# Kernel tuning notes

Measured on AMD Instinct MI355X. Metric: run time of the kernel, lower is better.

## Reference

```python
import jax, jax.numpy as jnp
import numpy as np

IN_CH, OUT_CH, HEAD, QK_DIM, V_DIM = 256, 256, 8, 512, 512


def setup_inputs() -> dict:
    key = jax.random.key(0)
    ks = jax.random.split(key, 5)
    B, H, W = 16, 32, 32
    x = jax.random.normal(ks[0], (B, IN_CH, H, W), dtype=jnp.float32)
    # 1x1 conv weights stored as [out_ch, in_ch]
    qkv_out = 2 * QK_DIM + V_DIM
    qkv_w = jax.random.normal(ks[1], (qkv_out, IN_CH), dtype=jnp.float32) * (IN_CH ** -0.5)
    qkv_b = jax.random.normal(ks[2], (qkv_out,), dtype=jnp.float32) * 0.02
    proj_w = jax.random.normal(ks[3], (OUT_CH, V_DIM), dtype=jnp.float32) * (V_DIM ** -0.5)
    proj_b = jax.random.normal(ks[4], (OUT_CH,), dtype=jnp.float32) * 0.02
    return {"x": x, "qkv_w": qkv_w, "qkv_b": qkv_b, "proj_w": proj_w, "proj_b": proj_b}


def reference(x, qkv_w, qkv_b, proj_w, proj_b):
    B, C, H, W = x.shape
    N = H * W
    dh = QK_DIM // HEAD
    dv = V_DIM // HEAD
    scale = dh ** -0.5
    # 1x1 conv == channel GEMM
    qkv = jnp.einsum('bchw,oc->bohw', x, qkv_w) + qkv_b[None, :, None, None]
    q, k, v = jnp.split(qkv, [QK_DIM, 2 * QK_DIM], axis=1)
    # [B, ch, H, W] -> [B, head, N, head_dim]
    def to_heads(t, d):
        return t.reshape(B, HEAD, d, N).transpose(0, 1, 3, 2)
    q = to_heads(q, dh)
    k = to_heads(k, dh)
    v = to_heads(v, dv)
    mask = jnp.tril(jnp.ones((N, N), dtype=bool))  # [N, N]
    scores = jnp.einsum('bhnd,bhmd->bhnm', q, k) * scale
    scores = jnp.where(mask, scores, -jnp.inf)
    attn = jax.nn.softmax(scores, axis=-1)
    attn = jnp.where(mask, attn, 0.0)
    out = jnp.einsum('bhnm,bhmd->bhnd', attn, v)  # [B, head, N, dv]
    out = out.transpose(0, 1, 3, 2).reshape(B, V_DIM, H, W)
    out = jnp.einsum('bvhw,ov->bohw', out, proj_w) + proj_b[None, :, None, None]
    return out
```

## Files before the change

### kernel.cpp

```cpp
#include <hip/hip_runtime.h>
#include <math.h>

static constexpr int Bsz = 16;
static constexpr int Np  = 1024;
static constexpr int Cin = 256;

typedef __attribute__((ext_vector_type(8))) short short8;
typedef __attribute__((ext_vector_type(4))) float f4;

#if defined(__has_builtin)
#if __has_builtin(__builtin_amdgcn_exp2f)
#define EXP2(x) __builtin_amdgcn_exp2f(x)
#else
#define EXP2(x) exp2f(x)
#endif
#else
#define EXP2(x) exp2f(x)
#endif

#define QSCALE 0.18033688011112f

__device__ __forceinline__ unsigned short f2b(float f) {
    union { float fp; unsigned int u; } v; v.fp = f;
    unsigned int r = v.u + 0x7fffu + ((v.u >> 16) & 1u);
    return (unsigned short)(r >> 16);
}

__device__ __forceinline__ unsigned cvtpk(float a, float b) {
    unsigned r;
    asm("v_cvt_pk_bf16_f32 %0, %1, %2" : "=v"(r) : "v"(a), "v"(b));
    return r;
}

__device__ __forceinline__ void* swzp(const void* base, int row, int col) {
    return (void*)((const char*)base + ((row * 128 + col * 2) ^ ((row & 7) << 4)));
}

__device__ __forceinline__ void gl16(const ushort* g, ushort* l) {
    __builtin_amdgcn_global_load_lds(
        (const __attribute__((address_space(1))) unsigned int*)g,
        (__attribute__((address_space(3))) unsigned int*)l, 16, 0, 0);
}

__global__ __launch_bounds__(256)
void cast_xw(const float* __restrict__ x, const float* __restrict__ qw,
             const float* __restrict__ pw, ushort* __restrict__ xb,
             ushort* __restrict__ qwb, ushort* __restrict__ pwb)
{
    const int t = threadIdx.x;
    if (blockIdx.y < 4) {
        __shared__ ushort T[64][72];
        const int n0 = blockIdx.x * 64, c0 = blockIdx.y * 64, b = blockIdx.z;
        {
            const int c_l = t >> 2, ns = (t & 3) * 16;
            const float* src = &x[((b * Cin + c0 + c_l) << 10) + n0 + ns];
#pragma unroll
            for (int i = 0; i < 4; ++i) {
                const float4 v = *(const float4*)(src + 4 * i);
                T[ns + 4 * i + 0][c_l] = f2b(v.x);
                T[ns + 4 * i + 1][c_l] = f2b(v.y);
                T[ns + 4 * i + 2][c_l] = f2b(v.z);
                T[ns + 4 * i + 3][c_l] = f2b(v.w);
            }
        }
        __syncthreads();
        {
            const int n_l = t >> 2, cs = (t & 3) * 16;
            ushort* dst = &xb[((b << 10) + n0 + n_l) * Cin + c0 + cs];
            *(uint4*)dst       = *(const uint4*)&T[n_l][cs];
            *(uint4*)(dst + 8) = *(const uint4*)&T[n_l][cs + 8];
        }
    } else {
        const int nq4 = (1536 * Cin) / 4;
        const int base = ((blockIdx.z * 16 + blockIdx.x) * 256 + t) * 2;
#pragma unroll
        for (int g = 0; g < 2; ++g) {
            const int j = base + g;
            const float* src; ushort* dst; int jj;
            if (j < nq4) { src = qw; dst = qwb; jj = j; }
            else         { src = pw; dst = pwb; jj = j - nq4; }
            const float4 v = *(const float4*)(src + 4 * jj);
            ushort4 u; u.x = f2b(v.x); u.y = f2b(v.y); u.z = f2b(v.z); u.w = f2b(v.w);
            *(ushort4*)(dst + 4 * jj) = u;
        }
    }
}

__global__ __launch_bounds__(256)
void qkv_gemm(const ushort* __restrict__ xb, const ushort* __restrict__ wb,
              const float* __restrict__ bias,
              ushort* __restrict__ qb, ushort* __restrict__ kb, ushort* __restrict__ vb)
{
    __shared__ ushort lds[17408];
    ushort* As = lds;
    ushort* Bs = lds + 8192;

    const int t = threadIdx.x;
    const int w = t >> 6, lane = t & 63, quad = lane >> 4, ln = lane & 15;
    const int n0 = blockIdx.x * 128;
    const int o0 = blockIdx.y * 128;
    const int b  = blockIdx.z;
    const int ow = (w & 1) * 64, nw = (w >> 1) * 64;
    const bool vpath = (o0 >= 1024);

    const int r8  = lane >> 3;
    const int c16 = ((lane & 7) ^ r8) << 3;

    f4 acc[4][4];
#pragma unroll
    for (int i = 0; i < 4; ++i)
#pragma unroll
        for (int j = 0; j < 4; ++j) acc[i][j] = (f4){0.f, 0.f, 0.f, 0.f};

    for (int k0 = 0; k0 < Cin; k0 += 64) {
        __syncthreads();
#pragma unroll
        for (int j = 0; j < 4; ++j) {
            const int row = w * 32 + j * 8 + r8;
            gl16(&wb[(o0 + row) * Cin + k0 + c16],              &As[(w * 32 + j * 8) * 64]);
            gl16(&xb[((b << 10) + n0 + row) * Cin + k0 + c16],  &Bs[(w * 32 + j * 8) * 64]);
        }
        __syncthreads();
#pragma unroll
        for (int sub = 0; sub < 2; ++sub) {
            short8 af[4], bf[4];
#pragma unroll
            for (int ot = 0; ot < 4; ++ot)
                af[ot] = *(const short8*)swzp(As, ow + ot * 16 + ln, sub * 32 + quad * 8);
#pragma unroll
            for (int nt = 0; nt < 4; ++nt)
                bf[nt] = *(const short8*)swzp(Bs, nw + nt * 16 + ln, sub * 32 + quad * 8);
            if (!vpath) {
#pragma unroll
                for (int ot = 0; ot < 4; ++ot)
#pragma unroll
                    for (int nt = 0; nt < 4; ++nt)
                        acc[ot][nt] = __builtin_amdgcn_mfma_f32_16x16x32_bf16(
                            af[ot], bf[nt], acc[ot][nt], 0, 0, 0);
            } else {
#pragma unroll
                for (int nt = 0; nt < 4; ++nt)
#pragma unroll
                    for (int ot = 0; ot < 4; ++ot)
                        acc[nt][ot] = __builtin_amdgcn_mfma_f32_16x16x32_bf16(
                            bf[nt], af[ot], acc[nt][ot], 0, 0, 0);
            }
        }
    }

    __syncthreads();
    if (!vpath) {
        ushort* Ct = lds;
        const float sc = (o0 < 512) ? QSCALE : 1.0f;
#pragma unroll
        for (int ot = 0; ot < 4; ++ot) {
            float bs[4];
#pragma unroll
            for (int rg = 0; rg < 4; ++rg)
                bs[rg] = bias[o0 + ow + ot * 16 + quad * 4 + rg];
#pragma unroll
            for (int nt = 0; nt < 4; ++nt) {
                ushort4 u;
                u.x = f2b((acc[ot][nt][0] + bs[0]) * sc);
                u.y = f2b((acc[ot][nt][1] + bs[1]) * sc);
                u.z = f2b((acc[ot][nt][2] + bs[2]) * sc);
                u.w = f2b((acc[ot][nt][3] + bs[3]) * sc);
                *(ushort4*)&Ct[(nw + nt * 16 + ln) * 136 + ow + ot * 16 + quad * 4] = u;
            }
        }
        __syncthreads();
        ushort* dst; int obase;
        if (o0 < 512) { dst = qb; obase = o0; }
        else          { dst = kb; obase = o0 - 512; }
        const int rn = t >> 1, hf = t & 1;
        const int bh = b * 8 + (obase >> 6) + hf;
        ushort* drow = &dst[(bh * Np + n0 + rn) << 6];
        const ushort* srow = &Ct[rn * 136 + hf * 64];
#pragma unroll
        for (int s = 0; s < 8; ++s)
            *(uint4*)(drow + s * 8) = *(const uint4*)(srow + s * 8);
    } else {
        ushort* Ct = lds;
#pragma unroll
        for (int ot = 0; ot < 4; ++ot) {
            const float bo = bias[o0 + ow + ot * 16 + ln];
#pragma unroll
            for (int nt = 0; nt < 4; ++nt) {
                ushort4 u;
                u.x = f2b(acc[nt][ot][0] + bo);
                u.y = f2b(acc[nt][ot][1] + bo);
                u.z = f2b(acc[nt][ot][2] + bo);
                u.w = f2b(acc[nt][ot][3] + bo);
                *(ushort4*)&Ct[(ow + ot * 16 + ln) * 136 + nw + nt * 16 + quad * 4] = u;
            }
        }
        __syncthreads();
        const int o_l = t >> 1, nh = (t & 1) * 64;
        const int bh = b * 8 + ((o0 - 1024) >> 6) + (o_l >> 6);
        ushort* drow = &vb[((size_t)bh << 16) + ((o_l & 63) << 10) + n0 + nh];
        const ushort* srow = &Ct[o_l * 136 + nh];
#pragma unroll
        for (int s = 0; s < 8; ++s)
            *(uint4*)(drow + s * 8) = *(const uint4*)(srow + s * 8);
    }
}

__global__ __launch_bounds__(256, 6)
void attn(const ushort* __restrict__ qb, const ushort* __restrict__ kb,
          const ushort* __restrict__ vt, ushort* __restrict__ ob)
{
    __shared__ ushort Ks[64 * 64];
    __shared__ ushort Vt[64 * 64];
    __shared__ ushort Ps[64 * 72];

    const int t    = threadIdx.x;
    const int w    = t >> 6;
    const int lane = t & 63;
    const int quad = lane >> 4;
    const int ln   = lane & 15;
    const int bh   = blockIdx.x & 127;
    const int qt   = 15 - (int)(blockIdx.x >> 7);
    const int q0   = qt * 64;

    const ushort* __restrict__ kbh = kb + ((size_t)(bh * Np) << 6);
    const ushort* __restrict__ vbh = vt + ((size_t)bh << 16);

    {
        const int r = t & 63, seg = t >> 6;
        const ushort* src = &qb[((size_t)(bh * Np + q0 + r) << 6) + seg * 16];
        *(uint4*)&Ps[r * 72 + seg * 16]     = *(const uint4*)src;
        *(uint4*)&Ps[r * 72 + seg * 16 + 8] = *(const uint4*)(src + 8);
    }
    __syncthreads();

    const short8 qa0 = *(const short8*)&Ps[(w * 16 + ln) * 72 + quad * 8];
    const short8 qa1 = *(const short8*)&Ps[(w * 16 + ln) * 72 + 32 + quad * 8];

    f4 o_[4];
#pragma unroll
    for (int nt = 0; nt < 4; ++nt) o_[nt] = (f4){0.f, 0.f, 0.f, 0.f};
    float m = -INFINITY, l = 0.f;

    const int r8  = lane >> 3;
    const int c16 = ((lane & 7) ^ r8) << 3;
    const int prow = (w * 16 + ln) * 72;
    const int qrow = q0 + w * 16 + ln;

    for (int kt = 0; kt <= qt; ++kt) {
        const int k0 = kt * 64;
        __syncthreads();
#pragma unroll
        for (int j = 0; j < 2; ++j) {
            const int ch  = w * 2 + j;
            const int row = ch * 8 + r8;
            gl16(&kbh[((k0 + row) << 6) + c16],               &Ks[ch * 512]);
            gl16(&vbh[((size_t)row << 10) + k0 + c16],        &Vt[ch * 512]);
        }
        __syncthreads();

        const bool diag = (kt == qt);

        f4 st[4];
#pragma unroll
        for (int mt = 0; mt < 4; ++mt) st[mt] = (f4){0.f, 0.f, 0.f, 0.f};
#pragma unroll
        for (int mt = 0; mt < 4; ++mt) {
            if (diag && mt > w) continue;
            const short8 ka0 = *(const short8*)swzp(Ks, mt * 16 + ln, quad * 8);
            const short8 ka1 = *(const short8*)swzp(Ks, mt * 16 + ln, 32 + quad * 8);
            st[mt] = __builtin_amdgcn_mfma_f32_16x16x32_bf16(ka0, qa0, st[mt], 0, 0, 0);
            st[mt] = __builtin_amdgcn_mfma_f32_16x16x32_bf16(ka1, qa1, st[mt], 0, 0, 0);
        }

        if (diag) {
#pragma unroll
            for (int mt = 0; mt < 4; ++mt)
#pragma unroll
                for (int rg = 0; rg < 4; ++rg)
                    if (k0 + mt * 16 + quad * 4 + rg > qrow) st[mt][rg] = -INFINITY;
        }

        float mx = st[0][0];
#pragma unroll
        for (int mt = 0; mt < 4; ++mt)
#pragma unroll
            for (int rg = 0; rg < 4; ++rg) mx = fmaxf(mx, st[mt][rg]);
        mx = fmaxf(mx, __shfl_xor(mx, 16));
        mx = fmaxf(mx, __shfl_xor(mx, 32));

        if (!__all(mx <= m + 8.f)) {
            const float mn = fmaxf(m, mx);
            const float al = EXP2(m - mn);
            m = mn; l *= al;
#pragma unroll
            for (int nt = 0; nt < 4; ++nt)
#pragma unroll
                for (int rg = 0; rg < 4; ++rg) o_[nt][rg] *= al;
        }

        float rs = 0.f;
#pragma unroll
        for (int mt = 0; mt < 4; ++mt) {
            const float p0 = EXP2(st[mt][0] - m);
            const float p1 = EXP2(st[mt][1] - m);
            const float p2 = EXP2(st[mt][2] - m);
            const float p3 = EXP2(st[mt][3] - m);
            rs += (p0 + p1) + (p2 + p3);
            uint2 u; u.x = cvtpk(p0, p1); u.y = cvtpk(p2, p3);
            *(uint2*)&Ps[prow + mt * 16 + quad * 4] = u;
        }
        rs += __shfl_xor(rs, 16);
        rs += __shfl_xor(rs, 32);
        l += rs;

#pragma unroll
        for (int ks = 0; ks < 2; ++ks) {
            if (diag && w * 16 + 15 < ks * 32) continue;
            const short8 pa = *(const short8*)&Ps[prow + ks * 32 + quad * 8];
#pragma unroll
            for (int nt = 0; nt < 4; ++nt) {
                const short8 vf = *(const short8*)swzp(Vt, nt * 16 + ln, ks * 32 + quad * 8);
                o_[nt] = __builtin_amdgcn_mfma_f32_16x16x32_bf16(vf, pa, o_[nt], 0, 0, 0);
            }
        }
    }

    const float li = 1.0f / l;
    ushort* orow = &ob[(size_t)(bh * Np + qrow) << 6];
#pragma unroll
    for (int nt = 0; nt < 4; ++nt) {
        uint2 u;
        u.x = cvtpk(o_[nt][0] * li, o_[nt][1] * li);
        u.y = cvtpk(o_[nt][2] * li, o_[nt][3] * li);
        *(uint2*)(orow + nt * 16 + quad * 4) = u;
    }
}

__global__ __launch_bounds__(256)
void proj_gemm(const ushort* __restrict__ obuf, const ushort* __restrict__ pwb,
               const float* __restrict__ bias, float* __restrict__ out)
{
    __shared__ ushort As[64 * 64];
    __shared__ ushort Bs[128 * 64];

    const int t = threadIdx.x;
    const int w = t >> 6, lane = t & 63, quad = lane >> 4, ln = lane & 15;
    const int n0 = blockIdx.x * 128;
    const int o0 = blockIdx.y * 64;
    const int b  = blockIdx.z;
    const int nw = w * 32;

    const int r8  = lane >> 3;
    const int c16 = ((lane & 7) ^ r8) << 3;

    f4 acc[4][2];
#pragma unroll
    for (int i = 0; i < 4; ++i)
#pragma unroll
        for (int j = 0; j < 2; ++j) acc[i][j] = (f4){0.f, 0.f, 0.f, 0.f};

    for (int k0 = 0; k0 < 512; k0 += 64) {
        __syncthreads();
        {
            const int head = k0 >> 6;
#pragma unroll
            for (int j = 0; j < 2; ++j) {
                const int ch = w * 2 + j, row = ch * 8 + r8;
                gl16(&pwb[(o0 + row) * 512 + k0 + c16], &As[ch * 512]);
            }
#pragma unroll
            for (int j = 0; j < 4; ++j) {
                const int ch = w * 4 + j, row = ch * 8 + r8;
                gl16(&obuf[(((b * 8 + head) * Np + n0 + row) << 6) + c16], &Bs[ch * 512]);
            }
        }
        __syncthreads();
#pragma unroll
        for (int sub = 0; sub < 2; ++sub) {
            short8 af[4], bf[2];
#pragma unroll
            for (int ot = 0; ot < 4; ++ot)
                af[ot] = *(const short8*)swzp(As, ot * 16 + ln, sub * 32 + quad * 8);
#pragma unroll
            for (int nt = 0; nt < 2; ++nt)
                bf[nt] = *(const short8*)swzp(Bs, nw + nt * 16 + ln, sub * 32 + quad * 8);
#pragma unroll
            for (int ot = 0; ot < 4; ++ot)
#pragma unroll
                for (int nt = 0; nt < 2; ++nt)
                    acc[ot][nt] = __builtin_amdgcn_mfma_f32_16x16x32_bf16(
                        af[ot], bf[nt], acc[ot][nt], 0, 0, 0);
        }
    }

#pragma unroll
    for (int ot = 0; ot < 4; ++ot) {
#pragma unroll
        for (int rg = 0; rg < 4; ++rg) {
            const int oo = o0 + ot * 16 + quad * 4 + rg;
            const float pb = bias[oo];
            float* drow = &out[((b << 8) + oo) << 10];
#pragma unroll
            for (int nt = 0; nt < 2; ++nt)
                drow[n0 + nw + nt * 16 + ln] = acc[ot][nt][rg] + pb;
        }
    }
}

extern "C" void kernel_launch(void* const* d_in, const int* in_sizes, int n_in,
                              void* d_out, int out_size, void* d_ws, size_t ws_size,
                              hipStream_t stream)
{
    const float* x   = (const float*)d_in[0];
    const float* qw  = (const float*)d_in[1];
    const float* qbb = (const float*)d_in[2];
    const float* pw  = (const float*)d_in[3];
    const float* pb  = (const float*)d_in[4];
    float* out = (float*)d_out;

    const size_t per = (size_t)Bsz * 8 * Np * 64;
    ushort* qbuf = (ushort*)d_ws;
    ushort* kbuf = qbuf + per;
    ushort* vbuf = kbuf + per;
    ushort* obuf = vbuf + per;
    ushort* xb   = obuf + per;
    ushort* qwb  = xb + (size_t)Bsz * Np * Cin;
    ushort* pwb  = qwb + 1536 * Cin;

    cast_xw<<<dim3(16, 5, Bsz), 256, 0, stream>>>(x, qw, pw, xb, qwb, pwb);
    qkv_gemm<<<dim3(8, 12, Bsz), 256, 0, stream>>>(xb, qwb, qbb, qbuf, kbuf, vbuf);
    attn<<<dim3(128 * 16), 256, 0, stream>>>(qbuf, kbuf, vbuf, obuf);
    proj_gemm<<<dim3(8, 4, Bsz), 256, 0, stream>>>(obuf, pwb, pb, out);
}
```

Baseline: 151.2 us.

## Double-buffer K/V tiles in attention and operand tiles in projection GEMM

Converts the attention kernel and the projection GEMM to double-buffered LDS. The next tile is prefetched with direct global-to-LDS loads while the current tile is computed, and one of the two barriers per iteration is dropped. The attention P/Q staging buffer switches from a padded layout to the swizzled layout, and attention launch bounds drop from 6 to 4 waves-per-SIMD hint because LDS use roughly doubles. This trades occupancy for overlap of memory latency with MFMA work.

```diff
diff --git a/kernel.cpp b/kernel.cpp
--- a/kernel.cpp
+++ b/kernel.cpp
@@ -205,13 +205,13 @@
     }
 }
 
-__global__ __launch_bounds__(256, 6)
+__global__ __launch_bounds__(256, 4)
 void attn(const ushort* __restrict__ qb, const ushort* __restrict__ kb,
           const ushort* __restrict__ vt, ushort* __restrict__ ob)
 {
-    __shared__ ushort Ks[64 * 64];
-    __shared__ ushort Vt[64 * 64];
-    __shared__ ushort Ps[64 * 72];
+    __shared__ ushort Ks[2][4096];
+    __shared__ ushort Vt[2][4096];
+    __shared__ ushort Ps[4096];
 
     const int t    = threadIdx.x;
     const int w    = t >> 6;
@@ -225,39 +225,45 @@
     const ushort* __restrict__ kbh = kb + ((size_t)(bh * Np) << 6);
     const ushort* __restrict__ vbh = vt + ((size_t)bh << 16);
 
+    const int r8  = lane >> 3;
+    const int c16 = ((lane & 7) ^ r8) << 3;
+
     {
-        const int r = t & 63, seg = t >> 6;
+        const int r = lane, seg = w;
         const ushort* src = &qb[((size_t)(bh * Np + q0 + r) << 6) + seg * 16];
-        *(uint4*)&Ps[r * 72 + seg * 16]     = *(const uint4*)src;
-        *(uint4*)&Ps[r * 72 + seg * 16 + 8] = *(const uint4*)(src + 8);
+        *(uint4*)swzp(Ps, r, seg * 16)     = *(const uint4*)src;
+        *(uint4*)swzp(Ps, r, seg * 16 + 8) = *(const uint4*)(src + 8);
+    }
+#pragma unroll
+    for (int j = 0; j < 2; ++j) {
+        const int ch = w * 2 + j, row = ch * 8 + r8;
+        gl16(&kbh[(row << 6) + c16],             &Ks[0][ch * 512]);
+        gl16(&vbh[((size_t)row << 10) + c16],    &Vt[0][ch * 512]);
     }
     __syncthreads();
 
-    const short8 qa0 = *(const short8*)&Ps[(w * 16 + ln) * 72 + quad * 8];
-    const short8 qa1 = *(const short8*)&Ps[(w * 16 + ln) * 72 + 32 + quad * 8];
+    const short8 qa0 = *(const short8*)swzp(Ps, w * 16 + ln, quad * 8);
+    const short8 qa1 = *(const short8*)swzp(Ps, w * 16 + ln, 32 + quad * 8);
 
     f4 o_[4];
 #pragma unroll
     for (int nt = 0; nt < 4; ++nt) o_[nt] = (f4){0.f, 0.f, 0.f, 0.f};
     float m = -INFINITY, l = 0.f;
-
-    const int r8  = lane >> 3;
-    const int c16 = ((lane & 7) ^ r8) << 3;
-    const int prow = (w * 16 + ln) * 72;
     const int qrow = q0 + w * 16 + ln;
 
     for (int kt = 0; kt <= qt; ++kt) {
+        const int cur = kt & 1;
+        if (kt < qt) {
+            const int nk0 = (kt + 1) * 64;
+#pragma unroll
+            for (int j = 0; j < 2; ++j) {
+                const int ch = w * 2 + j, row = ch * 8 + r8;
+                gl16(&kbh[((nk0 + row) << 6) + c16],          &Ks[cur ^ 1][ch * 512]);
+                gl16(&vbh[((size_t)row << 10) + nk0 + c16],   &Vt[cur ^ 1][ch * 512]);
+            }
+        }
+
         const int k0 = kt * 64;
-        __syncthreads();
-#pragma unroll
-        for (int j = 0; j < 2; ++j) {
-            const int ch  = w * 2 + j;
-            const int row = ch * 8 + r8;
-            gl16(&kbh[((k0 + row) << 6) + c16],               &Ks[ch * 512]);
-            gl16(&vbh[((size_t)row << 10) + k0 + c16],        &Vt[ch * 512]);
-        }
-        __syncthreads();
-
         const bool diag = (kt == qt);
 
         f4 st[4];
@@ -266,8 +272,8 @@
 #pragma unroll
         for (int mt = 0; mt < 4; ++mt) {
             if (diag && mt > w) continue;
-            const short8 ka0 = *(const short8*)swzp(Ks, mt * 16 + ln, quad * 8);
-            const short8 ka1 = *(const short8*)swzp(Ks, mt * 16 + ln, 32 + quad * 8);
+            const short8 ka0 = *(const short8*)swzp(Ks[cur], mt * 16 + ln, quad * 8);
+            const short8 ka1 = *(const short8*)swzp(Ks[cur], mt * 16 + ln, 32 + quad * 8);
             st[mt] = __builtin_amdgcn_mfma_f32_16x16x32_bf16(ka0, qa0, st[mt], 0, 0, 0);
             st[mt] = __builtin_amdgcn_mfma_f32_16x16x32_bf16(ka1, qa1, st[mt], 0, 0, 0);
         }
@@ -299,6 +305,7 @@
         }
 
         float rs = 0.f;
+        const int prow = w * 16 + ln;
 #pragma unroll
         for (int mt = 0; mt < 4; ++mt) {
             const float p0 = EXP2(st[mt][0] - m);
@@ -307,7 +314,7 @@
             const float p3 = EXP2(st[mt][3] - m);
             rs += (p0 + p1) + (p2 + p3);
             uint2 u; u.x = cvtpk(p0, p1); u.y = cvtpk(p2, p3);
-            *(uint2*)&Ps[prow + mt * 16 + quad * 4] = u;
+            *(uint2*)swzp(Ps, prow, mt * 16 + quad * 4) = u;
         }
         rs += __shfl_xor(rs, 16);
         rs += __shfl_xor(rs, 32);
@@ -316,13 +323,15 @@
 #pragma unroll
         for (int ks = 0; ks < 2; ++ks) {
             if (diag && w * 16 + 15 < ks * 32) continue;
-            const short8 pa = *(const short8*)&Ps[prow + ks * 32 + quad * 8];
+            const short8 pa = *(const short8*)swzp(Ps, prow, ks * 32 + quad * 8);
 #pragma unroll
             for (int nt = 0; nt < 4; ++nt) {
-                const short8 vf = *(const short8*)swzp(Vt, nt * 16 + ln, ks * 32 + quad * 8);
+                const short8 vf = *(const short8*)swzp(Vt[cur], nt * 16 + ln, ks * 32 + quad * 8);
                 o_[nt] = __builtin_amdgcn_mfma_f32_16x16x32_bf16(vf, pa, o_[nt], 0, 0, 0);
             }
         }
+
+        __syncthreads();
     }
 
     const float li = 1.0f / l;
@@ -340,8 +349,8 @@
 void proj_gemm(const ushort* __restrict__ obuf, const ushort* __restrict__ pwb,
                const float* __restrict__ bias, float* __restrict__ out)
 {
-    __shared__ ushort As[64 * 64];
-    __shared__ ushort Bs[128 * 64];
+    __shared__ ushort As[2][4096];
+    __shared__ ushort Bs[2][8192];
 
     const int t = threadIdx.x;
     const int w = t >> 6, lane = t & 63, quad = lane >> 4, ln = lane & 15;
@@ -359,31 +368,43 @@
 #pragma unroll
         for (int j = 0; j < 2; ++j) acc[i][j] = (f4){0.f, 0.f, 0.f, 0.f};
 
-    for (int k0 = 0; k0 < 512; k0 += 64) {
-        __syncthreads();
-        {
-            const int head = k0 >> 6;
+#pragma unroll
+    for (int j = 0; j < 2; ++j) {
+        const int ch = w * 2 + j, row = ch * 8 + r8;
+        gl16(&pwb[(o0 + row) * 512 + c16], &As[0][ch * 512]);
+    }
+#pragma unroll
+    for (int j = 0; j < 4; ++j) {
+        const int ch = w * 4 + j, row = ch * 8 + r8;
+        gl16(&obuf[(((b * 8 + 0) * Np + n0 + row) << 6) + c16], &Bs[0][ch * 512]);
+    }
+    __syncthreads();
+
+    for (int s = 0; s < 8; ++s) {
+        const int cur = s & 1;
+        if (s < 7) {
+            const int nk0 = (s + 1) * 64;
 #pragma unroll
             for (int j = 0; j < 2; ++j) {
                 const int ch = w * 2 + j, row = ch * 8 + r8;
-                gl16(&pwb[(o0 + row) * 512 + k0 + c16], &As[ch * 512]);
+                gl16(&pwb[(o0 + row) * 512 + nk0 + c16], &As[cur ^ 1][ch * 512]);
             }
 #pragma unroll
             for (int j = 0; j < 4; ++j) {
                 const int ch = w * 4 + j, row = ch * 8 + r8;
-                gl16(&obuf[(((b * 8 + head) * Np + n0 + row) << 6) + c16], &Bs[ch * 512]);
-            }
-        }
-        __syncthreads();
+                gl16(&obuf[(((b * 8 + s + 1) * Np + n0 + row) << 6) + c16],
+                     &Bs[cur ^ 1][ch * 512]);
+            }
+        }
 #pragma unroll
         for (int sub = 0; sub < 2; ++sub) {
             short8 af[4], bf[2];
 #pragma unroll
             for (int ot = 0; ot < 4; ++ot)
-                af[ot] = *(const short8*)swzp(As, ot * 16 + ln, sub * 32 + quad * 8);
+                af[ot] = *(const short8*)swzp(As[cur], ot * 16 + ln, sub * 32 + quad * 8);
 #pragma unroll
             for (int nt = 0; nt < 2; ++nt)
-                bf[nt] = *(const short8*)swzp(Bs, nw + nt * 16 + ln, sub * 32 + quad * 8);
+                bf[nt] = *(const short8*)swzp(Bs[cur], nw + nt * 16 + ln, sub * 32 + quad * 8);
 #pragma unroll
             for (int ot = 0; ot < 4; ++ot)
 #pragma unroll
@@ -391,6 +412,7 @@
                     acc[ot][nt] = __builtin_amdgcn_mfma_f32_16x16x32_bf16(
                         af[ot], bf[nt], acc[ot][nt], 0, 0, 0);
         }
+        __syncthreads();
     }
 
 #pragma unroll
```

Result: slower. 154.8 us (+2.4%).

## Read V fragments directly from global in attention; halve proj_gemm N-tile

Applied to the files above, without the earlier changes.

The attention kernel no longer stages V tiles into shared memory. Each wave loads its V fragments straight from global memory (transposed V layout) into MFMA operands, which frees LDS and allows the occupancy hint to rise from 6 to 8 blocks per CU. This drops one LDS tile and its barrier-covered copy, but every wave now issues redundant global loads for the same V data and relies on cache hits. Separately, proj_gemm's N tile is halved to 64 and the grid doubled, giving more blocks with less reuse per block.

```diff
diff --git a/kernel.cpp b/kernel.cpp
--- a/kernel.cpp
+++ b/kernel.cpp
@@ -205,12 +205,11 @@
     }
 }
 
-__global__ __launch_bounds__(256, 6)
+__global__ __launch_bounds__(256, 8)
 void attn(const ushort* __restrict__ qb, const ushort* __restrict__ kb,
           const ushort* __restrict__ vt, ushort* __restrict__ ob)
 {
     __shared__ ushort Ks[64 * 64];
-    __shared__ ushort Vt[64 * 64];
     __shared__ ushort Ps[64 * 72];
 
     const int t    = threadIdx.x;
@@ -253,8 +252,7 @@
         for (int j = 0; j < 2; ++j) {
             const int ch  = w * 2 + j;
             const int row = ch * 8 + r8;
-            gl16(&kbh[((k0 + row) << 6) + c16],               &Ks[ch * 512]);
-            gl16(&vbh[((size_t)row << 10) + k0 + c16],        &Vt[ch * 512]);
+            gl16(&kbh[((k0 + row) << 6) + c16], &Ks[ch * 512]);
         }
         __syncthreads();
 
@@ -316,10 +314,11 @@
 #pragma unroll
         for (int ks = 0; ks < 2; ++ks) {
             if (diag && w * 16 + 15 < ks * 32) continue;
+            const int kk = k0 + ks * 32;
             const short8 pa = *(const short8*)&Ps[prow + ks * 32 + quad * 8];
 #pragma unroll
             for (int nt = 0; nt < 4; ++nt) {
-                const short8 vf = *(const short8*)swzp(Vt, nt * 16 + ln, ks * 32 + quad * 8);
+                const short8 vf = *(const short8*)&vbh[(((size_t)(nt * 16 + ln)) << 10) + kk + quad * 8];
                 o_[nt] = __builtin_amdgcn_mfma_f32_16x16x32_bf16(vf, pa, o_[nt], 0, 0, 0);
             }
         }
@@ -341,23 +340,21 @@
                const float* __restrict__ bias, float* __restrict__ out)
 {
     __shared__ ushort As[64 * 64];
-    __shared__ ushort Bs[128 * 64];
+    __shared__ ushort Bs[64 * 64];
 
     const int t = threadIdx.x;
     const int w = t >> 6, lane = t & 63, quad = lane >> 4, ln = lane & 15;
-    const int n0 = blockIdx.x * 128;
+    const int n0 = blockIdx.x * 64;
     const int o0 = blockIdx.y * 64;
     const int b  = blockIdx.z;
-    const int nw = w * 32;
+    const int nw = w * 16;
 
     const int r8  = lane >> 3;
     const int c16 = ((lane & 7) ^ r8) << 3;
 
-    f4 acc[4][2];
-#pragma unroll
-    for (int i = 0; i < 4; ++i)
-#pragma unroll
-        for (int j = 0; j < 2; ++j) acc[i][j] = (f4){0.f, 0.f, 0.f, 0.f};
+    f4 acc[4];
+#pragma unroll
+    for (int i = 0; i < 4; ++i) acc[i] = (f4){0.f, 0.f, 0.f, 0.f};
 
     for (int k0 = 0; k0 < 512; k0 += 64) {
         __syncthreads();
@@ -367,29 +364,21 @@
             for (int j = 0; j < 2; ++j) {
                 const int ch = w * 2 + j, row = ch * 8 + r8;
                 gl16(&pwb[(o0 + row) * 512 + k0 + c16], &As[ch * 512]);
-            }
-#pragma unroll
-            for (int j = 0; j < 4; ++j) {
-                const int ch = w * 4 + j, row = ch * 8 + r8;
                 gl16(&obuf[(((b * 8 + head) * Np + n0 + row) << 6) + c16], &Bs[ch * 512]);
             }
         }
         __syncthreads();
 #pragma unroll
         for (int sub = 0; sub < 2; ++sub) {
-            short8 af[4], bf[2];
+            short8 af[4], bf;
 #pragma unroll
             for (int ot = 0; ot < 4; ++ot)
                 af[ot] = *(const short8*)swzp(As, ot * 16 + ln, sub * 32 + quad * 8);
-#pragma unroll
-            for (int nt = 0; nt < 2; ++nt)
-                bf[nt] = *(const short8*)swzp(Bs, nw + nt * 16 + ln, sub * 32 + quad * 8);
+            bf = *(const short8*)swzp(Bs, nw + ln, sub * 32 + quad * 8);
 #pragma unroll
             for (int ot = 0; ot < 4; ++ot)
-#pragma unroll
-                for (int nt = 0; nt < 2; ++nt)
-                    acc[ot][nt] = __builtin_amdgcn_mfma_f32_16x16x32_bf16(
-                        af[ot], bf[nt], acc[ot][nt], 0, 0, 0);
+                acc[ot] = __builtin_amdgcn_mfma_f32_16x16x32_bf16(
+                    af[ot], bf, acc[ot], 0, 0, 0);
         }
     }
 
@@ -400,9 +389,7 @@
             const int oo = o0 + ot * 16 + quad * 4 + rg;
             const float pb = bias[oo];
             float* drow = &out[((b << 8) + oo) << 10];
-#pragma unroll
-            for (int nt = 0; nt < 2; ++nt)
-                drow[n0 + nw + nt * 16 + ln] = acc[ot][nt][rg] + pb;
+            drow[n0 + nw + ln] = acc[ot][rg] + pb;
         }
     }
 }
@@ -430,5 +417,5 @@
     cast_xw<<<dim3(16, 5, Bsz), 256, 0, stream>>>(x, qw, pw, xb, qwb, pwb);
     qkv_gemm<<<dim3(8, 12, Bsz), 256, 0, stream>>>(xb, qwb, qbb, qbuf, kbuf, vbuf);
     attn<<<dim3(128 * 16), 256, 0, stream>>>(qbuf, kbuf, vbuf, obuf);
-    proj_gemm<<<dim3(8, 4, Bsz), 256, 0, stream>>>(obuf, pwb, pb, out);
-}
+    proj_gemm<<<dim3(16, 4, Bsz), 256, 0, stream>>>(obuf, pwb, pb, out);
+}
```

Result: slower. 196.9 us (+30.2%).
